# Kernel tuning notes

Hardware: AMD Instinct MI355X
Metric: run time of the kernel (lower is better)

## Reference

```python
import jax, jax.numpy as jnp
import numpy as np

N_NODES = 50000
N_EDGES = 600000
IN_FEAT = 128
OUT_FEAT = 128
NUM_RELS = 8


def setup_inputs() -> dict:
    key = jax.random.key(0)
    ks = jax.random.split(key, 8)
    h = jax.random.normal(ks[0], (N_NODES, IN_FEAT), dtype=jnp.float32)
    # xavier_uniform-like scale for relation weights
    limit = float(np.sqrt(6.0 / (IN_FEAT + OUT_FEAT)))
    weight = jax.random.uniform(ks[1], (NUM_RELS, IN_FEAT, OUT_FEAT), jnp.float32, -limit, limit)
    limit_g = float(np.sqrt(6.0 / (IN_FEAT + 1)))
    gate_weight = jax.random.uniform(ks[2], (NUM_RELS, IN_FEAT, 1), jnp.float32, -limit_g, limit_g)
    h_bias = jnp.zeros((OUT_FEAT,), jnp.float32)
    loop_weight = jax.random.uniform(ks[3], (IN_FEAT, OUT_FEAT), jnp.float32, -limit, limit)
    norm = jax.random.uniform(ks[4], (N_EDGES, 1), jnp.float32)
    src = jax.random.randint(ks[5], (N_EDGES,), 0, N_NODES, dtype=jnp.int32)
    dst = jax.random.randint(ks[6], (N_EDGES,), 0, N_NODES, dtype=jnp.int32)
    rel_type = jax.random.randint(ks[7], (N_EDGES,), 0, NUM_RELS, dtype=jnp.int32)
    return {"h": h, "weight": weight, "gate_weight": gate_weight, "h_bias": h_bias,
            "loop_weight": loop_weight, "norm": norm, "src": src, "dst": dst,
            "rel_type": rel_type}


def reference(h, weight, gate_weight, h_bias, loop_weight, norm, src, dst, rel_type):
    n_nodes = h.shape[0]
    # Transform all nodes under every relation once ([R, N, out]); cheaper than
    # materializing per-edge [E, in, out] weight gathers for small R.
    h_rel = jnp.einsum('ni,rio->rno', h, weight)          # [R, N, out]
    msg = h_rel[rel_type, src]                             # [E, out] gather
    msg = msg * norm                                       # per-edge norm
    # relation-specific scalar gate on src features
    gate_rel = jnp.einsum('ni,ri->rn', h, gate_weight[:, :, 0])  # [R, N]
    gate = jax.nn.sigmoid(gate_rel[rel_type, src])[:, None]      # [E, 1]
    msg = msg * gate
    # scatter-sum messages into destination nodes
    agg = jax.ops.segment_sum(msg, dst, num_segments=n_nodes)    # [N, out]
    out = agg + h_bias + h @ loop_weight                   # bias + self-loop
    out = jax.nn.relu(out)                                 # activation
    # dropout p=0.0 (deterministic) -> identity
    return out
```

## Files before the change

### kernel.cpp

```cpp
#include <hip/hip_runtime.h>

#define N_NODES 50000
#define N_EDGES 600000
#define F 128
#define NRELL 9
#define NB_SCAN 196
#define NB2 1563

#define WT3_OFF   0
#define H2_OFF    294912
#define GATE3_OFF 13094912
#define CNT3_OFF  14694912
#define EXCL3_OFF 16294912
#define BSUM3_OFF 17895168
#define REC3_OFF  17901568
#define A3_OFF    22701568
#define WS_NEED3  ((size_t)138012160)

#define GATE_OFF   294912
#define HREL_OFF   1894912
#define HREL_BYTES (9ll*N_NODES*128*2)
#define CNT_OFF    117094912
#define BASE_OFF   117294912
#define CUR_OFF    117494912
#define BSUM_OFF   117694912
#define SORT_OFF   117695936
#define WS_NEED2   ((size_t)120095936)
#define WS_NEED1   ((size_t)HREL_OFF + (size_t)HREL_BYTES)

typedef __attribute__((ext_vector_type(8))) short short8;
typedef __attribute__((ext_vector_type(4))) float floatx4;

__device__ inline unsigned short f32_to_bf16(float f) {
    unsigned u = __float_as_uint(f);
    unsigned r = u + 0x7fff + ((u >> 16) & 1);
    return (unsigned short)(r >> 16);
}
__device__ inline float bf16_to_f32(unsigned short s) {
    return __uint_as_float(((unsigned)s) << 16);
}
__device__ inline float bf16lo(unsigned m) { return __uint_as_float(m << 16); }
__device__ inline float bf16hi(unsigned m) { return __uint_as_float(m & 0xffff0000u); }
__device__ inline float sigmoidf(float x) { return 1.f / (1.f + __expf(-x)); }

__global__ void k_prep_w(const float* __restrict__ W, const float* __restrict__ LW,
                         unsigned short* __restrict__ Wt, int swz) {
    int idx = blockIdx.x * 256 + threadIdx.x;
    if (idx >= 9 * 128 * 128) return;
    int r = idx >> 14;
    int rem = idx & 16383;
    int i = rem >> 7, o = rem & 127;
    float v = (r < 8) ? W[(r << 14) + (i << 7) + o] : LW[(i << 7) + o];
    int pos;
    if (swz) {
        int g = (i >> 3) ^ (o & 7);
        pos = (r << 14) + (o << 7) + (g << 3) + (i & 7);
    } else {
        pos = (r << 14) + (o << 7) + i;
    }
    Wt[pos] = f32_to_bf16(v);
}

__global__ void k_prep_h(const float* __restrict__ h, const float* __restrict__ gw,
                         unsigned short* __restrict__ h2, float* __restrict__ gate) {
    int wave = threadIdx.x >> 6, lane = threadIdx.x & 63;
    int n = blockIdx.x * 4 + wave;
    float2 hv = *(const float2*)(h + (size_t)n * F + lane * 2);
    unsigned val = (unsigned)f32_to_bf16(hv.x) | ((unsigned)f32_to_bf16(hv.y) << 16);
    *(unsigned*)(h2 + (size_t)n * F + lane * 2) = val;
    #pragma unroll
    for (int r = 0; r < 8; ++r) {
        float2 wv = *(const float2*)(gw + r * F + lane * 2);
        float p = hv.x * wv.x + hv.y * wv.y;
        #pragma unroll
        for (int off = 32; off; off >>= 1) p += __shfl_xor(p, off);
        if (lane == 0) gate[r * N_NODES + n] = sigmoidf(p);
    }
}

__global__ void k_hist2(const int* __restrict__ dst, const int* __restrict__ rel,
                        int* __restrict__ cnt) {
    int e = blockIdx.x * 256 + threadIdx.x;
    if (e < N_EDGES) atomicAdd(&cnt[dst[e] * 8 + rel[e]], 1);
}

__global__ void k_s1(const int* __restrict__ cnt, int* __restrict__ excl,
                     int* __restrict__ bsum) {
    __shared__ int sh[256];
    int g = blockIdx.x * 256 + threadIdx.x;
    int v = (g < 400000) ? cnt[g] : 0;
    sh[threadIdx.x] = v;
    __syncthreads();
    #pragma unroll
    for (int off = 1; off < 256; off <<= 1) {
        int t = (threadIdx.x >= off) ? sh[threadIdx.x - off] : 0;
        __syncthreads();
        sh[threadIdx.x] += t;
        __syncthreads();
    }
    if (g < 400000) excl[g] = sh[threadIdx.x] - v;
    if (threadIdx.x == 255) bsum[blockIdx.x] = sh[255];
}

__global__ void k_s2(int* __restrict__ bsum) {
    __shared__ int sh[256];
    int t = threadIdx.x;
    int v[7];
    int s = 0;
    #pragma unroll
    for (int j = 0; j < 7; ++j) {
        int idx = t * 7 + j;
        v[j] = (idx < NB2) ? bsum[idx] : 0;
        s += v[j];
    }
    sh[t] = s;
    __syncthreads();
    #pragma unroll
    for (int off = 1; off < 256; off <<= 1) {
        int tt = (t >= off) ? sh[t - off] : 0;
        __syncthreads();
        sh[t] += tt;
        __syncthreads();
    }
    int run = sh[t] - s;
    #pragma unroll
    for (int j = 0; j < 7; ++j) {
        int idx = t * 7 + j;
        if (idx < NB2) bsum[idx] = run;
        run += v[j];
    }
}

__global__ void k_s3(int* __restrict__ excl, const int* __restrict__ bsum,
                     int* __restrict__ cursor) {
    int g = blockIdx.x * 256 + threadIdx.x;
    if (g < 400000) {
        int b = excl[g] + bsum[blockIdx.x];
        excl[g] = b;
        cursor[g] = b;
    }
    if (g == 0) excl[400000] = N_EDGES;
}

__global__ void k_scatter2(const int* __restrict__ src, const int* __restrict__ dst,
                           const int* __restrict__ rel, const float* __restrict__ norm,
                           const float* __restrict__ gate, int* __restrict__ cursor,
                           int2* __restrict__ rec) {
    int e = blockIdx.x * 256 + threadIdx.x;
    if (e >= N_EDGES) return;
    int d = dst[e], r = rel[e], s = src[e];
    int pos = atomicAdd(&cursor[d * 8 + r], 1);
    float sc = norm[e] * gate[r * N_NODES + s];
    rec[pos] = make_int2(s, __float_as_int(sc));
}

__global__ __launch_bounds__(256) void k_aggA(const unsigned short* __restrict__ h2,
                                              const int2* __restrict__ rec,
                                              const int* __restrict__ excl,
                                              unsigned short* __restrict__ A) {
    int wave = threadIdx.x >> 6, lane = threadIdx.x & 63;
    int n = blockIdx.x * 4 + wave;
    int ex = 0;
    if (lane < 9) ex = excl[n * 8 + lane];
    int e0 = __shfl(ex, 0), e8 = __shfl(ex, 8);
    int deg = e8 - e0;
    unsigned short* Arow = A + (size_t)n * 1152;
    int swo = (((lane >> 2) ^ (n & 7)) << 2) + (lane & 3);

    if (deg <= 64) {
        int rs = 0; float rsc = 0.f;
        if (lane < deg) {
            int2 rc = rec[e0 + lane];
            rs = rc.x; rsc = __int_as_float(rc.y);
        }
        for (int r = 0; r < 8; ++r) {
            int s = __shfl(ex, r) - e0;
            int e = __shfl(ex, r + 1) - e0;
            float a0 = 0.f, a1 = 0.f;
            for (int j = s; j < e; ++j) {
                int sj = __shfl(rs, j);
                float sc = __shfl(rsc, j);
                unsigned m = *(const unsigned*)(h2 + (size_t)sj * F + lane * 2);
                a0 += sc * bf16lo(m);
                a1 += sc * bf16hi(m);
            }
            unsigned val = (unsigned)f32_to_bf16(a0) | ((unsigned)f32_to_bf16(a1) << 16);
            ((unsigned*)(Arow + r * 128))[swo] = val;
        }
    } else {
        for (int r = 0; r < 8; ++r) {
            int s = __shfl(ex, r);
            int e = __shfl(ex, r + 1);
            float a0 = 0.f, a1 = 0.f;
            for (int idx = s; idx < e; ++idx) {
                int2 rc = rec[idx];
                float sc = __int_as_float(rc.y);
                unsigned m = *(const unsigned*)(h2 + (size_t)rc.x * F + lane * 2);
                a0 += sc * bf16lo(m);
                a1 += sc * bf16hi(m);
            }
            unsigned val = (unsigned)f32_to_bf16(a0) | ((unsigned)f32_to_bf16(a1) << 16);
            ((unsigned*)(Arow + r * 128))[swo] = val;
        }
    }
    unsigned hm = ((const unsigned*)(h2 + (size_t)n * F))[lane];
    ((unsigned*)(Arow + 8 * 128))[swo] = hm;
}

__global__ __launch_bounds__(256) void k_gemmA(const unsigned short* __restrict__ A,
                                               const unsigned short* __restrict__ Wt,
                                               const float* __restrict__ bias,
                                               float* __restrict__ out) {
    __shared__ unsigned short sA[16384];
    __shared__ unsigned short sB[16384];
    int tid = threadIdx.x;
    int nb = blockIdx.x * 128;
    int wave = tid >> 6, lane = tid & 63, lrow = lane & 15, quad = lane >> 4;

    floatx4 acc[2][8];
    #pragma unroll
    for (int mt = 0; mt < 2; ++mt)
        #pragma unroll
        for (int nt = 0; nt < 8; ++nt) acc[mt][nt] = (floatx4){0.f, 0.f, 0.f, 0.f};

    for (int kb = 0; kb < 9; ++kb) {
        __syncthreads();
        #pragma unroll
        for (int it = 0; it < 8; ++it) {
            int g = it * 256 + tid;
            int row = g >> 4, gr = g & 15;
            *(uint4*)(&sA[row * 128 + gr * 8]) =
                *(const uint4*)(A + (size_t)(nb + row) * 1152 + kb * 128 + gr * 8);
            *(uint4*)(&sB[row * 128 + gr * 8]) =
                *(const uint4*)(Wt + (kb << 14) + (g << 3));
        }
        __syncthreads();
        #pragma unroll
        for (int kt = 0; kt < 4; ++kt) {
            int j = kt * 4 + quad;
            int sw = (j ^ (lrow & 7)) << 3;
            short8 a0 = *(const short8*)(&sA[(wave * 32 + lrow) * 128 + sw]);
            short8 a1 = *(const short8*)(&sA[(wave * 32 + 16 + lrow) * 128 + sw]);
            #pragma unroll
            for (int nt = 0; nt < 8; ++nt) {
                short8 b = *(const short8*)(&sB[(nt * 16 + lrow) * 128 + sw]);
                acc[0][nt] = __builtin_amdgcn_mfma_f32_16x16x32_bf16(a0, b, acc[0][nt], 0, 0, 0);
                acc[1][nt] = __builtin_amdgcn_mfma_f32_16x16x32_bf16(a1, b, acc[1][nt], 0, 0, 0);
            }
        }
    }
    #pragma unroll
    for (int mt = 0; mt < 2; ++mt) {
        #pragma unroll
        for (int nt = 0; nt < 8; ++nt) {
            int col = nt * 16 + lrow;
            float bv = bias[col];
            #pragma unroll
            for (int g = 0; g < 4; ++g) {
                int row = nb + wave * 32 + mt * 16 + quad * 4 + g;
                if (row < N_NODES)
                    out[(size_t)row * F + col] = fmaxf(acc[mt][nt][g] + bv, 0.f);
            }
        }
    }
}

__global__ void k_gate(const float* __restrict__ h, const float* __restrict__ gw,
                       float* __restrict__ gate) {
    int wave = threadIdx.x >> 6, lane = threadIdx.x & 63;
    int n = blockIdx.x * 4 + wave;
    if (n >= N_NODES) return;
    float2 hv = *(const float2*)(h + (size_t)n * F + lane * 2);
    #pragma unroll
    for (int r = 0; r < 8; ++r) {
        float2 wv = *(const float2*)(gw + r * F + lane * 2);
        float p = hv.x * wv.x + hv.y * wv.y;
        #pragma unroll
        for (int off = 32; off; off >>= 1) p += __shfl_xor(p, off);
        if (lane == 0) gate[r * N_NODES + n] = sigmoidf(p);
    }
}

#define LDH 136
#define LDW 136
__global__ __launch_bounds__(256) void k_hrel(const float* __restrict__ h,
                                              const unsigned short* __restrict__ Wt,
                                              unsigned short* __restrict__ hrel) {
    __shared__ unsigned short hA[64 * LDH];
    __shared__ unsigned short wB[128 * LDW];
    int tid = threadIdx.x;
    int nb = blockIdx.x * 64;
    #pragma unroll
    for (int it = 0; it < 8; ++it) {
        int idx = it * 1024 + tid * 4;
        int row = idx >> 7, col = idx & 127;
        int node = nb + row;
        float4 v;
        if (node < N_NODES) v = *(const float4*)(h + (size_t)node * F + col);
        else                v = make_float4(0.f, 0.f, 0.f, 0.f);
        ushort4 b;
        b.x = f32_to_bf16(v.x); b.y = f32_to_bf16(v.y);
        b.z = f32_to_bf16(v.z); b.w = f32_to_bf16(v.w);
        *(ushort4*)(&hA[row * LDH + col]) = b;
    }
    int wave = tid >> 6, lane = tid & 63;
    int lrow = lane & 15, quad = lane >> 4;
    const unsigned short* aptr = &hA[(wave * 16 + lrow) * LDH + quad * 8];
    for (int r = 0; r < NRELL; ++r) {
        __syncthreads();
        #pragma unroll
        for (int it = 0; it < 8; ++it) {
            int idx = it * 2048 + tid * 8;
            int o = idx >> 7, i = idx & 127;
            *(uint4*)(&wB[o * LDW + i]) = *(const uint4*)(Wt + (r << 14) + idx);
        }
        __syncthreads();
        floatx4 acc[8];
        #pragma unroll
        for (int nt = 0; nt < 8; ++nt) acc[nt] = (floatx4){0.f, 0.f, 0.f, 0.f};
        #pragma unroll
        for (int kt = 0; kt < 4; ++kt) {
            short8 a = *(const short8*)(aptr + kt * 32);
            #pragma unroll
            for (int nt = 0; nt < 8; ++nt) {
                short8 b = *(const short8*)(&wB[(nt * 16 + lrow) * LDW + kt * 32 + quad * 8]);
                acc[nt] = __builtin_amdgcn_mfma_f32_16x16x32_bf16(a, b, acc[nt], 0, 0, 0);
            }
        }
        unsigned short* dstp = hrel + (size_t)r * N_NODES * F;
        #pragma unroll
        for (int nt = 0; nt < 8; ++nt) {
            #pragma unroll
            for (int g = 0; g < 4; ++g) {
                int node = nb + wave * 16 + quad * 4 + g;
                if (node < N_NODES)
                    dstp[(size_t)node * F + nt * 16 + lrow] = f32_to_bf16(acc[nt][g]);
            }
        }
    }
}

__global__ void k_hist(const int* __restrict__ dst, int* __restrict__ cnt) {
    int e = blockIdx.x * 256 + threadIdx.x;
    if (e < N_EDGES) atomicAdd(&cnt[dst[e]], 1);
}

__global__ void k_scan1(const int* __restrict__ cnt, int* __restrict__ excl,
// ... 105 lines not shown
    float v1 = bf16hi(m) * scale;
    float* op = out + (size_t)d * F + lane * 2;
    unsafeAtomicAdd(op, v0);
    unsafeAtomicAdd(op + 1, v1);
}

__global__ void k_final(float* __restrict__ out, const float* __restrict__ bias,
                        const unsigned short* __restrict__ hrel8) {
    int idx = blockIdx.x * 256 + threadIdx.x;
    if (idx >= N_NODES * 32) return;
    int node = idx >> 5, c4 = (idx & 31) * 4;
    float4 a = *(float4*)(out + (size_t)node * F + c4);
    float4 b = *(const float4*)(bias + c4);
    ushort4 l = *(const ushort4*)(hrel8 + (size_t)node * F + c4);
    float o0 = fmaxf(a.x + b.x + bf16_to_f32(l.x), 0.f);
    float o1 = fmaxf(a.y + b.y + bf16_to_f32(l.y), 0.f);
    float o2 = fmaxf(a.z + b.z + bf16_to_f32(l.z), 0.f);
    float o3 = fmaxf(a.w + b.w + bf16_to_f32(l.w), 0.f);
    *(float4*)(out + (size_t)node * F + c4) = make_float4(o0, o1, o2, o3);
}

__global__ void k_edges_fb(const float* __restrict__ h, const float* __restrict__ W,
                           const float* __restrict__ gw, const float* __restrict__ norm,
                           const int* __restrict__ src, const int* __restrict__ dst,
                           const int* __restrict__ rel, float* __restrict__ out) {
    int wave = threadIdx.x >> 6, lane = threadIdx.x & 63;
    int e = blockIdx.x * 4 + wave;
    if (e >= N_EDGES) return;
    int s = src[e], d = dst[e], r = rel[e];
    float2 hv = *(const float2*)(h + (size_t)s * F + lane * 2);
    float2 gv = *(const float2*)(gw + r * F + lane * 2);
    float p = hv.x * gv.x + hv.y * gv.y;
    #pragma unroll
    for (int off = 32; off; off >>= 1) p += __shfl_xor(p, off);
    float scale = norm[e] * sigmoidf(p);
    const float* wr = W + ((size_t)r << 14);
    float a0 = 0.f, a1 = 0.f;
    for (int i2 = 0; i2 < 64; ++i2) {
        float x0 = __shfl(hv.x, i2), x1 = __shfl(hv.y, i2);
        a0 += x0 * wr[(2 * i2) * F + lane]      + x1 * wr[(2 * i2 + 1) * F + lane];
        a1 += x0 * wr[(2 * i2) * F + 64 + lane] + x1 * wr[(2 * i2 + 1) * F + 64 + lane];
    }
    unsafeAtomicAdd(out + (size_t)d * F + lane,      a0 * scale);
    unsafeAtomicAdd(out + (size_t)d * F + 64 + lane, a1 * scale);
}

__global__ void k_final_fb(const float* __restrict__ h, const float* __restrict__ LW,
                           const float* __restrict__ bias, float* __restrict__ out) {
    int wave = threadIdx.x >> 6, lane = threadIdx.x & 63;
    int n = blockIdx.x * 4 + wave;
    if (n >= N_NODES) return;
    float2 hv = *(const float2*)(h + (size_t)n * F + lane * 2);
    float a0 = 0.f, a1 = 0.f;
    for (int i2 = 0; i2 < 64; ++i2) {
        float x0 = __shfl(hv.x, i2), x1 = __shfl(hv.y, i2);
        a0 += x0 * LW[(2 * i2) * F + lane]      + x1 * LW[(2 * i2 + 1) * F + lane];
        a1 += x0 * LW[(2 * i2) * F + 64 + lane] + x1 * LW[(2 * i2 + 1) * F + 64 + lane];
    }
    float* op = out + (size_t)n * F;
    op[lane]      = fmaxf(op[lane]      + bias[lane]      + a0, 0.f);
    op[64 + lane] = fmaxf(op[64 + lane] + bias[64 + lane] + a1, 0.f);
}

extern "C" void kernel_launch(void* const* d_in, const int* in_sizes, int n_in,
                              void* d_out, int out_size, void* d_ws, size_t ws_size,
                              hipStream_t stream) {
    const float* h    = (const float*)d_in[0];
    const float* W    = (const float*)d_in[1];
    const float* gw   = (const float*)d_in[2];
    const float* bias = (const float*)d_in[3];
    const float* lw   = (const float*)d_in[4];
    const float* norm = (const float*)d_in[5];
    const int* src    = (const int*)d_in[6];
    const int* dst    = (const int*)d_in[7];
    const int* rel    = (const int*)d_in[8];
    float* out = (float*)d_out;

    if (ws_size >= WS_NEED3) {
        unsigned short* Wt   = (unsigned short*)((char*)d_ws + WT3_OFF);
        unsigned short* h2   = (unsigned short*)((char*)d_ws + H2_OFF);
        float*          gate = (float*)((char*)d_ws + GATE3_OFF);
        int*            cnt  = (int*)((char*)d_ws + CNT3_OFF);
        int*            excl = (int*)((char*)d_ws + EXCL3_OFF);
        int*            bsum = (int*)((char*)d_ws + BSUM3_OFF);
        int2*           rec  = (int2*)((char*)d_ws + REC3_OFF);
        unsigned short* A    = (unsigned short*)((char*)d_ws + A3_OFF);

        hipMemsetAsync(cnt, 0, 400000 * sizeof(int), stream);
        k_prep_w<<<576, 256, 0, stream>>>(W, lw, Wt, 1);
        k_prep_h<<<12500, 256, 0, stream>>>(h, gw, h2, gate);
        k_hist2<<<2344, 256, 0, stream>>>(dst, rel, cnt);
        k_s1<<<NB2, 256, 0, stream>>>(cnt, excl, bsum);
        k_s2<<<1, 256, 0, stream>>>(bsum);
        k_s3<<<NB2, 256, 0, stream>>>(excl, bsum, cnt);
        k_scatter2<<<2344, 256, 0, stream>>>(src, dst, rel, norm, gate, cnt, rec);
        k_aggA<<<12500, 256, 0, stream>>>(h2, rec, excl, A);
        k_gemmA<<<391, 256, 0, stream>>>(A, Wt, bias, out);
    } else if (ws_size >= WS_NEED2) {
        unsigned short* Wt   = (unsigned short*)d_ws;
        float*          gate = (float*)((char*)d_ws + GATE_OFF);
        unsigned short* hrel = (unsigned short*)((char*)d_ws + HREL_OFF);
        int* cnt    = (int*)((char*)d_ws + CNT_OFF);
        int* base   = (int*)((char*)d_ws + BASE_OFF);
        int* cursor = (int*)((char*)d_ws + CUR_OFF);
        int* bsum   = (int*)((char*)d_ws + BSUM_OFF);
        int* sorted = (int*)((char*)d_ws + SORT_OFF);
        hipMemsetAsync(cnt, 0, N_NODES * sizeof(int), stream);
        k_prep_w<<<576, 256, 0, stream>>>(W, lw, Wt, 0);
        k_gate<<<12500, 256, 0, stream>>>(h, gw, gate);
        k_hist<<<2344, 256, 0, stream>>>(dst, cnt);
        k_scan1<<<NB_SCAN, 256, 0, stream>>>(cnt, base, bsum);
        k_scan2<<<1, 256, 0, stream>>>(bsum);
        k_scan3<<<NB_SCAN, 256, 0, stream>>>(base, bsum, cursor);
        k_scatter<<<2344, 256, 0, stream>>>(dst, cursor, sorted);
        k_hrel<<<782, 256, 0, stream>>>(h, Wt, hrel);
        k_agg<<<12500, 256, 0, stream>>>(hrel, gate, norm, src, rel, sorted,
                                         base, cnt, bias, out);
    } else if (ws_size >= WS_NEED1) {
        unsigned short* Wt   = (unsigned short*)d_ws;
        float*          gate = (float*)((char*)d_ws + GATE_OFF);
        unsigned short* hrel = (unsigned short*)((char*)d_ws + HREL_OFF);
        hipMemsetAsync(d_out, 0, (size_t)out_size * sizeof(float), stream);
        k_prep_w<<<576, 256, 0, stream>>>(W, lw, Wt, 0);
        k_gate<<<12500, 256, 0, stream>>>(h, gw, gate);
        k_hrel<<<782, 256, 0, stream>>>(h, Wt, hrel);
        k_edges<<<150000, 256, 0, stream>>>(hrel, gate, norm, src, dst, rel, out);
        k_final<<<6250, 256, 0, stream>>>(out, bias, hrel + (size_t)8 * N_NODES * F);
    } else {
        hipMemsetAsync(d_out, 0, (size_t)out_size * sizeof(float), stream);
        k_edges_fb<<<150000, 256, 0, stream>>>(h, W, gw, norm, src, dst, rel, out);
        k_final_fb<<<12500, 256, 0, stream>>>(h, lw, bias, out);
    }
}
```

Measured before the change: 272.0 us.

## Fuse prep kernels with memset and replace three-pass scan with single-pass decoupled scan

Folds the count memset, weight conversion and node conversion/gate kernels into one multi-role launch that also zeroes the scan metadata. Replaces the three-kernel block scan (local scan, single-block bsum scan, add-back) with one 49-block chained scan. That scan takes block ids from an atomic ticket and passes prefixes between blocks through flag words, spin-waiting on the previous block. The goal is fewer launches and fewer passes over the 400K-entry count array, at the cost of a serial inter-block chain across only 49 blocks.

```diff
diff --git a/kernel.cpp b/kernel.cpp
--- a/kernel.cpp
+++ b/kernel.cpp
@@ -6,6 +6,7 @@
 #define NRELL 9
 #define NB_SCAN 196
 #define NB2 1563
+#define SCB 49
 
 #define WT3_OFF   0
 #define H2_OFF    294912
@@ -42,6 +43,240 @@
 __device__ inline float bf16lo(unsigned m) { return __uint_as_float(m << 16); }
 __device__ inline float bf16hi(unsigned m) { return __uint_as_float(m & 0xffff0000u); }
 __device__ inline float sigmoidf(float x) { return 1.f / (1.f + __expf(-x)); }
+__device__ inline unsigned packbf(float a0, float a1) {
+    return (unsigned)f32_to_bf16(a0) | ((unsigned)f32_to_bf16(a1) << 16);
+}
+
+__global__ __launch_bounds__(256) void k_prep(
+    const float* __restrict__ h, const float* __restrict__ W,
+    const float* __restrict__ gw, const float* __restrict__ lw,
+    unsigned short* __restrict__ Wt, unsigned short* __restrict__ h2,
+    float* __restrict__ gate, int* __restrict__ cnt, int* __restrict__ meta)
+{
+    int vb = blockIdx.x, tid = threadIdx.x;
+    if (vb < 391) {
+        int idx = vb * 1024 + tid * 4;
+        if (idx < 400000) *(int4*)(cnt + idx) = make_int4(0, 0, 0, 0);
+    } else if (vb == 391) {
+        meta[tid] = 0;
+    } else if (vb < 968) {
+        int idx = (vb - 392) * 256 + tid;
+        int r = idx >> 14, rem = idx & 16383, i = rem >> 7, o = rem & 127;
+        float v = (r < 8) ? W[(r << 14) + (i << 7) + o] : lw[(i << 7) + o];
+        int g = (i >> 3) ^ (o & 7);
+        Wt[(r << 14) + (o << 7) + (g << 3) + (i & 7)] = f32_to_bf16(v);
+    } else {
+        int wave = tid >> 6, lane = tid & 63;
+        int n = (vb - 968) * 4 + wave;
+        float2 hv = *(const float2*)(h + (size_t)n * F + lane * 2);
+        *(unsigned*)(h2 + (size_t)n * F + lane * 2) = packbf(hv.x, hv.y);
+        #pragma unroll
+        for (int r = 0; r < 8; ++r) {
+            float2 wv = *(const float2*)(gw + r * F + lane * 2);
+            float p = hv.x * wv.x + hv.y * wv.y;
+            #pragma unroll
+            for (int off = 32; off; off >>= 1) p += __shfl_xor(p, off);
+            if (lane == 0) gate[r * N_NODES + n] = sigmoidf(p);
+        }
+    }
+}
+
+__global__ void k_hist2(const int* __restrict__ dst, const int* __restrict__ rel,
+                        int* __restrict__ cnt) {
+    int e = blockIdx.x * 256 + threadIdx.x;
+    if (e < N_EDGES) atomicAdd(&cnt[dst[e] * 8 + rel[e]], 1);
+}
+
+__global__ __launch_bounds__(256) void k_scan(int* __restrict__ cnt,
+                                              int* __restrict__ excl,
+                                              int* __restrict__ meta) {
+    __shared__ int sh[256];
+    __shared__ int sbid, sprefix;
+    int tid = threadIdx.x;
+    if (tid == 0) sbid = atomicAdd(&meta[0], 1);
+    __syncthreads();
+    int bid = sbid;
+    int* flagsum = meta + 16;
+
+    int g0 = bid * 8192 + tid * 32;
+    int vals[32];
+    #pragma unroll
+    for (int j = 0; j < 8; ++j) {
+        int idx = g0 + j * 4;
+        int4 v = (idx + 3 < 400000) ? *(const int4*)(cnt + idx)
+                                    : make_int4(idx < 400000 ? cnt[idx] : 0,
+                                                idx + 1 < 400000 ? cnt[idx + 1] : 0,
+                                                idx + 2 < 400000 ? cnt[idx + 2] : 0,
+                                                idx + 3 < 400000 ? cnt[idx + 3] : 0);
+        vals[j * 4] = v.x; vals[j * 4 + 1] = v.y; vals[j * 4 + 2] = v.z; vals[j * 4 + 3] = v.w;
+    }
+    int run = 0;
+    #pragma unroll
+    for (int j = 0; j < 32; ++j) { int e = run; run += vals[j]; vals[j] = e; }
+    int tsum = run;
+
+    sh[tid] = tsum;
+    __syncthreads();
+    #pragma unroll
+    for (int off = 1; off < 256; off <<= 1) {
+        int t = (tid >= off) ? sh[tid - off] : 0;
+        __syncthreads();
+        sh[tid] += t;
+        __syncthreads();
+    }
+    int texcl = sh[tid] - tsum;
+    int btot = sh[255];
+
+    if (tid == 0) {
+        int prefix = 0;
+        if (bid > 0) {
+            int f;
+            do {
+                f = __hip_atomic_load(&flagsum[bid - 1], __ATOMIC_ACQUIRE,
+                                      __HIP_MEMORY_SCOPE_AGENT);
+                if (f == 0) __builtin_amdgcn_s_sleep(1);
+            } while (f == 0);
+            prefix = f - 1;
+        }
+        sprefix = prefix;
+        __hip_atomic_store(&flagsum[bid], prefix + btot + 1, __ATOMIC_RELEASE,
+                           __HIP_MEMORY_SCOPE_AGENT);
+    }
+    __syncthreads();
+    int p = sprefix + texcl;
+
+    #pragma unroll
+    for (int j = 0; j < 32; ++j) {
+        int idx = g0 + j;
+        if (idx < 400000) {
+            int b = p + vals[j];
+            excl[idx] = b;
+            cnt[idx] = b;
+        }
+    }
+    if (bid == SCB - 1 && tid == 0) excl[400000] = N_EDGES;
+}
+
+__global__ void k_scatter2(const int* __restrict__ src, const int* __restrict__ dst,
+                           const int* __restrict__ rel, const float* __restrict__ norm,
+                           const float* __restrict__ gate, int* __restrict__ cursor,
+                           int2* __restrict__ rec) {
+    int e = blockIdx.x * 256 + threadIdx.x;
+    if (e >= N_EDGES) return;
+    int d = dst[e], r = rel[e], s = src[e];
+    int pos = atomicAdd(&cursor[d * 8 + r], 1);
+    float sc = norm[e] * gate[r * N_NODES + s];
+    rec[pos] = make_int2(s, __float_as_int(sc));
+}
+
+__global__ __launch_bounds__(256) void k_aggA(const unsigned short* __restrict__ h2,
+                                              const int2* __restrict__ rec,
+                                              const int* __restrict__ excl,
+                                              unsigned short* __restrict__ A) {
+    int wave = threadIdx.x >> 6, lane = threadIdx.x & 63;
+    int n = blockIdx.x * 4 + wave;
+    int ex = 0;
+    if (lane < 9) ex = excl[n * 8 + lane];
+    int e0 = __shfl(ex, 0), e8 = __shfl(ex, 8);
+    int deg = e8 - e0;
+    unsigned short* Arow = A + (size_t)n * 1152;
+    int swo = (((lane >> 2) ^ (n & 7)) << 2) + (lane & 3);
+
+    if (deg <= 64) {
+        int rs = 0; float rsc = 0.f;
+        if (lane < deg) {
+            int2 rc = rec[e0 + lane];
+            rs = rc.x; rsc = __int_as_float(rc.y);
+        }
+        for (int r = 0; r < 8; ++r) {
+            int s = __shfl(ex, r) - e0;
+            int e = __shfl(ex, r + 1) - e0;
+            float a0 = 0.f, a1 = 0.f;
+            for (int j = s; j < e; ++j) {
+                int sj = __shfl(rs, j);
+                float sc = __shfl(rsc, j);
+                unsigned m = *(const unsigned*)(h2 + (size_t)sj * F + lane * 2);
+                a0 += sc * bf16lo(m);
+                a1 += sc * bf16hi(m);
+            }
+            ((unsigned*)(Arow + r * 128))[swo] = packbf(a0, a1);
+        }
+    } else {
+        for (int r = 0; r < 8; ++r) {
+            int s = __shfl(ex, r);
+            int e = __shfl(ex, r + 1);
+            float a0 = 0.f, a1 = 0.f;
+            for (int idx = s; idx < e; ++idx) {
+                int2 rc = rec[idx];
+                float sc = __int_as_float(rc.y);
+                unsigned m = *(const unsigned*)(h2 + (size_t)rc.x * F + lane * 2);
+                a0 += sc * bf16lo(m);
+                a1 += sc * bf16hi(m);
+            }
+            ((unsigned*)(Arow + r * 128))[swo] = packbf(a0, a1);
+        }
+    }
+    unsigned hm = ((const unsigned*)(h2 + (size_t)n * F))[lane];
+    ((unsigned*)(Arow + 8 * 128))[swo] = hm;
+}
+
+__global__ __launch_bounds__(256) void k_gemmA(const unsigned short* __restrict__ A,
+                                               const unsigned short* __restrict__ Wt,
+                                               const float* __restrict__ bias,
+                                               float* __restrict__ out) {
+    __shared__ unsigned short sA[16384];
+    __shared__ unsigned short sB[16384];
+    int tid = threadIdx.x;
+    int nb = blockIdx.x * 128;
+    int wave = tid >> 6, lane = tid & 63, lrow = lane & 15, quad = lane >> 4;
+
+    floatx4 acc[2][8];
+    #pragma unroll
+    for (int mt = 0; mt < 2; ++mt)
+        #pragma unroll
+        for (int nt = 0; nt < 8; ++nt) acc[mt][nt] = (floatx4){0.f, 0.f, 0.f, 0.f};
+
+    for (int kb = 0; kb < 9; ++kb) {
+        __syncthreads();
+        #pragma unroll
+        for (int it = 0; it < 8; ++it) {
+            int g = it * 256 + tid;
+            int row = g >> 4, gr = g & 15;
+            *(uint4*)(&sA[row * 128 + gr * 8]) =
+                *(const uint4*)(A + (size_t)(nb + row) * 1152 + kb * 128 + gr * 8);
+            *(uint4*)(&sB[row * 128 + gr * 8]) =
+                *(const uint4*)(Wt + (kb << 14) + (g << 3));
+        }
+        __syncthreads();
+        #pragma unroll
+        for (int kt = 0; kt < 4; ++kt) {
+            int j = kt * 4 + quad;
+            int sw = (j ^ (lrow & 7)) << 3;
+            short8 a0 = *(const short8*)(&sA[(wave * 32 + lrow) * 128 + sw]);
+            short8 a1 = *(const short8*)(&sA[(wave * 32 + 16 + lrow) * 128 + sw]);
+            #pragma unroll
+            for (int nt = 0; nt < 8; ++nt) {
+                short8 b = *(const short8*)(&sB[(nt * 16 + lrow) * 128 + sw]);
+                acc[0][nt] = __builtin_amdgcn_mfma_f32_16x16x32_bf16(a0, b, acc[0][nt], 0, 0, 0);
+                acc[1][nt] = __builtin_amdgcn_mfma_f32_16x16x32_bf16(a1, b, acc[1][nt], 0, 0, 0);
+            }
+        }
+    }
+    #pragma unroll
+    for (int mt = 0; mt < 2; ++mt) {
+        #pragma unroll
+        for (int nt = 0; nt < 8; ++nt) {
+            int col = nt * 16 + lrow;
+            float bv = bias[col];
+            #pragma unroll
+            for (int g = 0; g < 4; ++g) {
+                int row = nb + wave * 32 + mt * 16 + quad * 4 + g;
+                if (row < N_NODES)
+                    out[(size_t)row * F + col] = fmaxf(acc[mt][nt][g] + bv, 0.f);
+            }
+        }
+    }
+}
 
 __global__ void k_prep_w(const float* __restrict__ W, const float* __restrict__ LW,
                          unsigned short* __restrict__ Wt, int swz) {
@@ -59,210 +294,6 @@
         pos = (r << 14) + (o << 7) + i;
     }
     Wt[pos] = f32_to_bf16(v);
-}
-
-__global__ void k_prep_h(const float* __restrict__ h, const float* __restrict__ gw,
-                         unsigned short* __restrict__ h2, float* __restrict__ gate) {
-    int wave = threadIdx.x >> 6, lane = threadIdx.x & 63;
-    int n = blockIdx.x * 4 + wave;
-    float2 hv = *(const float2*)(h + (size_t)n * F + lane * 2);
-    unsigned val = (unsigned)f32_to_bf16(hv.x) | ((unsigned)f32_to_bf16(hv.y) << 16);
-    *(unsigned*)(h2 + (size_t)n * F + lane * 2) = val;
-    #pragma unroll
-    for (int r = 0; r < 8; ++r) {
-        float2 wv = *(const float2*)(gw + r * F + lane * 2);
-        float p = hv.x * wv.x + hv.y * wv.y;
-        #pragma unroll
-        for (int off = 32; off; off >>= 1) p += __shfl_xor(p, off);
-        if (lane == 0) gate[r * N_NODES + n] = sigmoidf(p);
-    }
-}
-
-__global__ void k_hist2(const int* __restrict__ dst, const int* __restrict__ rel,
-                        int* __restrict__ cnt) {
-    int e = blockIdx.x * 256 + threadIdx.x;
-    if (e < N_EDGES) atomicAdd(&cnt[dst[e] * 8 + rel[e]], 1);
-}
-
-__global__ void k_s1(const int* __restrict__ cnt, int* __restrict__ excl,
-                     int* __restrict__ bsum) {
-    __shared__ int sh[256];
-    int g = blockIdx.x * 256 + threadIdx.x;
-    int v = (g < 400000) ? cnt[g] : 0;
-    sh[threadIdx.x] = v;
-    __syncthreads();
-    #pragma unroll
-    for (int off = 1; off < 256; off <<= 1) {
-        int t = (threadIdx.x >= off) ? sh[threadIdx.x - off] : 0;
-        __syncthreads();
-        sh[threadIdx.x] += t;
-        __syncthreads();
-    }
-    if (g < 400000) excl[g] = sh[threadIdx.x] - v;
-    if (threadIdx.x == 255) bsum[blockIdx.x] = sh[255];
-}
-
-__global__ void k_s2(int* __restrict__ bsum) {
-    __shared__ int sh[256];
-    int t = threadIdx.x;
-    int v[7];
-    int s = 0;
-    #pragma unroll
-    for (int j = 0; j < 7; ++j) {
-        int idx = t * 7 + j;
-        v[j] = (idx < NB2) ? bsum[idx] : 0;
-        s += v[j];
-    }
-    sh[t] = s;
-    __syncthreads();
-    #pragma unroll
-    for (int off = 1; off < 256; off <<= 1) {
-        int tt = (t >= off) ? sh[t - off] : 0;
-        __syncthreads();
-        sh[t] += tt;
-        __syncthreads();
-    }
-    int run = sh[t] - s;
-    #pragma unroll
-    for (int j = 0; j < 7; ++j) {
-        int idx = t * 7 + j;
-        if (idx < NB2) bsum[idx] = run;
-        run += v[j];
-    }
-}
-
-__global__ void k_s3(int* __restrict__ excl, const int* __restrict__ bsum,
-                     int* __restrict__ cursor) {
-    int g = blockIdx.x * 256 + threadIdx.x;
-    if (g < 400000) {
-        int b = excl[g] + bsum[blockIdx.x];
-        excl[g] = b;
-        cursor[g] = b;
-    }
-    if (g == 0) excl[400000] = N_EDGES;
-}
-
-__global__ void k_scatter2(const int* __restrict__ src, const int* __restrict__ dst,
-                           const int* __restrict__ rel, const float* __restrict__ norm,
-                           const float* __restrict__ gate, int* __restrict__ cursor,
-                           int2* __restrict__ rec) {
-    int e = blockIdx.x * 256 + threadIdx.x;
-    if (e >= N_EDGES) return;
-    int d = dst[e], r = rel[e], s = src[e];
-    int pos = atomicAdd(&cursor[d * 8 + r], 1);
-    float sc = norm[e] * gate[r * N_NODES + s];
-    rec[pos] = make_int2(s, __float_as_int(sc));
-}
-
-__global__ __launch_bounds__(256) void k_aggA(const unsigned short* __restrict__ h2,
-                                              const int2* __restrict__ rec,
-                                              const int* __restrict__ excl,
-                                              unsigned short* __restrict__ A) {
-    int wave = threadIdx.x >> 6, lane = threadIdx.x & 63;
-    int n = blockIdx.x * 4 + wave;
-    int ex = 0;
-    if (lane < 9) ex = excl[n * 8 + lane];
-    int e0 = __shfl(ex, 0), e8 = __shfl(ex, 8);
-    int deg = e8 - e0;
-    unsigned short* Arow = A + (size_t)n * 1152;
-    int swo = (((lane >> 2) ^ (n & 7)) << 2) + (lane & 3);
-
-    if (deg <= 64) {
-        int rs = 0; float rsc = 0.f;
-        if (lane < deg) {
-            int2 rc = rec[e0 + lane];
-            rs = rc.x; rsc = __int_as_float(rc.y);
-        }
-        for (int r = 0; r < 8; ++r) {
-            int s = __shfl(ex, r) - e0;
-            int e = __shfl(ex, r + 1) - e0;
-            float a0 = 0.f, a1 = 0.f;
-            for (int j = s; j < e; ++j) {
-                int sj = __shfl(rs, j);
-                float sc = __shfl(rsc, j);
-                unsigned m = *(const unsigned*)(h2 + (size_t)sj * F + lane * 2);
-                a0 += sc * bf16lo(m);
-                a1 += sc * bf16hi(m);
-            }
-            unsigned val = (unsigned)f32_to_bf16(a0) | ((unsigned)f32_to_bf16(a1) << 16);
-            ((unsigned*)(Arow + r * 128))[swo] = val;
-        }
-    } else {
-        for (int r = 0; r < 8; ++r) {
-            int s = __shfl(ex, r);
-            int e = __shfl(ex, r + 1);
-            float a0 = 0.f, a1 = 0.f;
-            for (int idx = s; idx < e; ++idx) {
-                int2 rc = rec[idx];
-                float sc = __int_as_float(rc.y);
-                unsigned m = *(const unsigned*)(h2 + (size_t)rc.x * F + lane * 2);
-                a0 += sc * bf16lo(m);
-                a1 += sc * bf16hi(m);
-            }
-            unsigned val = (unsigned)f32_to_bf16(a0) | ((unsigned)f32_to_bf16(a1) << 16);
-            ((unsigned*)(Arow + r * 128))[swo] = val;
-        }
-    }
-    unsigned hm = ((const unsigned*)(h2 + (size_t)n * F))[lane];
-    ((unsigned*)(Arow + 8 * 128))[swo] = hm;
-}
-
-__global__ __launch_bounds__(256) void k_gemmA(const unsigned short* __restrict__ A,
-                                               const unsigned short* __restrict__ Wt,
-                                               const float* __restrict__ bias,
-                                               float* __restrict__ out) {
-    __shared__ unsigned short sA[16384];
-    __shared__ unsigned short sB[16384];
-    int tid = threadIdx.x;
-    int nb = blockIdx.x * 128;
-    int wave = tid >> 6, lane = tid & 63, lrow = lane & 15, quad = lane >> 4;
-
-    floatx4 acc[2][8];
-    #pragma unroll
-    for (int mt = 0; mt < 2; ++mt)
-        #pragma unroll
-        for (int nt = 0; nt < 8; ++nt) acc[mt][nt] = (floatx4){0.f, 0.f, 0.f, 0.f};
-
-    for (int kb = 0; kb < 9; ++kb) {
-        __syncthreads();
-        #pragma unroll
-        for (int it = 0; it < 8; ++it) {
-            int g = it * 256 + tid;
-            int row = g >> 4, gr = g & 15;
-            *(uint4*)(&sA[row * 128 + gr * 8]) =
-                *(const uint4*)(A + (size_t)(nb + row) * 1152 + kb * 128 + gr * 8);
-            *(uint4*)(&sB[row * 128 + gr * 8]) =
-                *(const uint4*)(Wt + (kb << 14) + (g << 3));
-        }
-        __syncthreads();
-        #pragma unroll
-        for (int kt = 0; kt < 4; ++kt) {
-            int j = kt * 4 + quad;
-            int sw = (j ^ (lrow & 7)) << 3;
-            short8 a0 = *(const short8*)(&sA[(wave * 32 + lrow) * 128 + sw]);
-            short8 a1 = *(const short8*)(&sA[(wave * 32 + 16 + lrow) * 128 + sw]);
-            #pragma unroll
-            for (int nt = 0; nt < 8; ++nt) {
-                short8 b = *(const short8*)(&sB[(nt * 16 + lrow) * 128 + sw]);
-                acc[0][nt] = __builtin_amdgcn_mfma_f32_16x16x32_bf16(a0, b, acc[0][nt], 0, 0, 0);
-                acc[1][nt] = __builtin_amdgcn_mfma_f32_16x16x32_bf16(a1, b, acc[1][nt], 0, 0, 0);
-            }
-        }
-    }
-    #pragma unroll
-    for (int mt = 0; mt < 2; ++mt) {
-        #pragma unroll
-        for (int nt = 0; nt < 8; ++nt) {
-            int col = nt * 16 + lrow;
-            float bv = bias[col];
-            #pragma unroll
-            for (int g = 0; g < 4; ++g) {
-                int row = nb + wave * 32 + mt * 16 + quad * 4 + g;
-                if (row < N_NODES)
-                    out[(size_t)row * F + col] = fmaxf(acc[mt][nt][g] + bv, 0.f);
-            }
-        }
-    }
 }
 
 __global__ void k_gate(const float* __restrict__ h, const float* __restrict__ gw,
@@ -534,17 +565,13 @@
         float*          gate = (float*)((char*)d_ws + GATE3_OFF);
         int*            cnt  = (int*)((char*)d_ws + CNT3_OFF);
         int*            excl = (int*)((char*)d_ws + EXCL3_OFF);
-        int*            bsum = (int*)((char*)d_ws + BSUM3_OFF);
+        int*            meta = (int*)((char*)d_ws + BSUM3_OFF);
         int2*           rec  = (int2*)((char*)d_ws + REC3_OFF);
         unsigned short* A    = (unsigned short*)((char*)d_ws + A3_OFF);
 
-        hipMemsetAsync(cnt, 0, 400000 * sizeof(int), stream);
-        k_prep_w<<<576, 256, 0, stream>>>(W, lw, Wt, 1);
-        k_prep_h<<<12500, 256, 0, stream>>>(h, gw, h2, gate);
+        k_prep<<<13468, 256, 0, stream>>>(h, W, gw, lw, Wt, h2, gate, cnt, meta);
         k_hist2<<<2344, 256, 0, stream>>>(dst, rel, cnt);
-        k_s1<<<NB2, 256, 0, stream>>>(cnt, excl, bsum);
-        k_s2<<<1, 256, 0, stream>>>(bsum);
-        k_s3<<<NB2, 256, 0, stream>>>(excl, bsum, cnt);
+        k_scan<<<SCB, 256, 0, stream>>>(cnt, excl, meta);
         k_scatter2<<<2344, 256, 0, stream>>>(src, dst, rel, norm, gate, cnt, rec);
         k_aggA<<<12500, 256, 0, stream>>>(h2, rec, excl, A);
         k_gemmA<<<391, 256, 0, stream>>>(A, Wt, bias, out);
```

Measured after the change: 318.9 us. 17.2% more time.

## Fuse prep kernels, transpose gate layout, read self-loop features directly in GEMM

Applied to the files above, without the earlier changes.

Merges weight conversion, bf16 feature conversion with gate computation, and the edge histogram into one launch that branches on block index, removing two kernel launches. The gate table moves from relation-major to node-major, so each node's eight gates are stored contiguously and scatter reads per source node are local. The aggregation kernel no longer copies each node's own features into a ninth slot of A, and the GEMM loads the self-loop tile straight from h2 with an on-the-fly swizzle. This shrinks the A buffer and the workspace requirement, at the cost of a branch in the GEMM load loop.

```diff
diff --git a/kernel.cpp b/kernel.cpp
--- a/kernel.cpp
+++ b/kernel.cpp
@@ -15,7 +15,7 @@
 #define BSUM3_OFF 17895168
 #define REC3_OFF  17901568
 #define A3_OFF    22701568
-#define WS_NEED3  ((size_t)138012160)
+#define WS_NEED3  ((size_t)125199872)
 
 #define GATE_OFF   294912
 #define HREL_OFF   1894912
@@ -42,6 +42,234 @@
 __device__ inline float bf16lo(unsigned m) { return __uint_as_float(m << 16); }
 __device__ inline float bf16hi(unsigned m) { return __uint_as_float(m & 0xffff0000u); }
 __device__ inline float sigmoidf(float x) { return 1.f / (1.f + __expf(-x)); }
+__device__ inline unsigned packbf(float a0, float a1) {
+    return (unsigned)f32_to_bf16(a0) | ((unsigned)f32_to_bf16(a1) << 16);
+}
+
+__global__ __launch_bounds__(256) void k_prep(
+    const float* __restrict__ h, const float* __restrict__ W,
+    const float* __restrict__ gw, const float* __restrict__ lw,
+    const int* __restrict__ dst, const int* __restrict__ rel,
+    unsigned short* __restrict__ Wt, unsigned short* __restrict__ h2,
+    float* __restrict__ gate, int* __restrict__ cnt)
+{
+    int vb = blockIdx.x, tid = threadIdx.x;
+    if (vb < 576) {
+        int idx = vb * 256 + tid;
+        int r = idx >> 14, rem = idx & 16383, i = rem >> 7, o = rem & 127;
+        float v = (r < 8) ? W[(r << 14) + (i << 7) + o] : lw[(i << 7) + o];
+        int g = (i >> 3) ^ (o & 7);
+        Wt[(r << 14) + (o << 7) + (g << 3) + (i & 7)] = f32_to_bf16(v);
+    } else if (vb < 13076) {
+        int wave = tid >> 6, lane = tid & 63;
+        int n = (vb - 576) * 4 + wave;
+        float2 hv = *(const float2*)(h + (size_t)n * F + lane * 2);
+        *(unsigned*)(h2 + (size_t)n * F + lane * 2) = packbf(hv.x, hv.y);
+        float g = 0.f;
+        #pragma unroll
+        for (int r = 0; r < 8; ++r) {
+            float2 wv = *(const float2*)(gw + r * F + lane * 2);
+            float p = hv.x * wv.x + hv.y * wv.y;
+            #pragma unroll
+            for (int off = 32; off; off >>= 1) p += __shfl_xor(p, off);
+            if (lane == r) g = sigmoidf(p);
+        }
+        if (lane < 8) gate[(size_t)n * 8 + lane] = g;
+    } else {
+        int e = (vb - 13076) * 256 + tid;
+        if (e < N_EDGES) atomicAdd(&cnt[dst[e] * 8 + rel[e]], 1);
+    }
+}
+
+__global__ void k_s1(const int* __restrict__ cnt, int* __restrict__ excl,
+                     int* __restrict__ bsum) {
+    __shared__ int sh[256];
+    int g = blockIdx.x * 256 + threadIdx.x;
+    int v = (g < 400000) ? cnt[g] : 0;
+    sh[threadIdx.x] = v;
+    __syncthreads();
+    #pragma unroll
+    for (int off = 1; off < 256; off <<= 1) {
+        int t = (threadIdx.x >= off) ? sh[threadIdx.x - off] : 0;
+        __syncthreads();
+        sh[threadIdx.x] += t;
+        __syncthreads();
+    }
+    if (g < 400000) excl[g] = sh[threadIdx.x] - v;
+    if (threadIdx.x == 255) bsum[blockIdx.x] = sh[255];
+}
+
+__global__ void k_s2(int* __restrict__ bsum) {
+    __shared__ int sh[256];
+    int t = threadIdx.x;
+    int v[7];
+    int s = 0;
+    #pragma unroll
+    for (int j = 0; j < 7; ++j) {
+        int idx = t * 7 + j;
+        v[j] = (idx < NB2) ? bsum[idx] : 0;
+        s += v[j];
+    }
+    sh[t] = s;
+    __syncthreads();
+    #pragma unroll
+    for (int off = 1; off < 256; off <<= 1) {
+        int tt = (t >= off) ? sh[t - off] : 0;
+        __syncthreads();
+        sh[t] += tt;
+        __syncthreads();
+    }
+    int run = sh[t] - s;
+    #pragma unroll
+    for (int j = 0; j < 7; ++j) {
+        int idx = t * 7 + j;
+        if (idx < NB2) bsum[idx] = run;
+        run += v[j];
+    }
+}
+
+__global__ void k_s3(int* __restrict__ excl, const int* __restrict__ bsum,
+                     int* __restrict__ cursor) {
+    int g = blockIdx.x * 256 + threadIdx.x;
+    if (g < 400000) {
+        int b = excl[g] + bsum[blockIdx.x];
+        excl[g] = b;
+        cursor[g] = b;
+    }
+    if (g == 0) excl[400000] = N_EDGES;
+}
+
+__global__ void k_scatter2(const int* __restrict__ src, const int* __restrict__ dst,
+                           const int* __restrict__ rel, const float* __restrict__ norm,
+                           const float* __restrict__ gate, int* __restrict__ cursor,
+                           int2* __restrict__ rec) {
+    int e = blockIdx.x * 256 + threadIdx.x;
+    if (e >= N_EDGES) return;
+    int d = dst[e], r = rel[e], s = src[e];
+    int pos = atomicAdd(&cursor[d * 8 + r], 1);
+    float sc = norm[e] * gate[(size_t)s * 8 + r];
+    rec[pos] = make_int2(s, __float_as_int(sc));
+}
+
+__global__ __launch_bounds__(256) void k_aggA(const unsigned short* __restrict__ h2,
+                                              const int2* __restrict__ rec,
+                                              const int* __restrict__ excl,
+                                              unsigned short* __restrict__ A) {
+    int wave = threadIdx.x >> 6, lane = threadIdx.x & 63;
+    int n = blockIdx.x * 4 + wave;
+    int ex = 0;
+    if (lane < 9) ex = excl[n * 8 + lane];
+    int e0 = __shfl(ex, 0), e8 = __shfl(ex, 8);
+    int deg = e8 - e0;
+    unsigned short* Arow = A + (size_t)n * 1024;
+    int swo = (((lane >> 2) ^ (n & 7)) << 2) + (lane & 3);
+
+    if (deg <= 64) {
+        int rs = 0; float rsc = 0.f;
+        if (lane < deg) {
+            int2 rc = rec[e0 + lane];
+            rs = rc.x; rsc = __int_as_float(rc.y);
+        }
+        for (int r = 0; r < 8; ++r) {
+            int s = __shfl(ex, r) - e0;
+            int e = __shfl(ex, r + 1) - e0;
+            float a0 = 0.f, a1 = 0.f;
+            for (int j = s; j < e; ++j) {
+                int sj = __shfl(rs, j);
+                float sc = __shfl(rsc, j);
+                unsigned m = *(const unsigned*)(h2 + (size_t)sj * F + lane * 2);
+                a0 += sc * bf16lo(m);
+                a1 += sc * bf16hi(m);
+            }
+            ((unsigned*)(Arow + r * 128))[swo] = packbf(a0, a1);
+        }
+    } else {
+        for (int r = 0; r < 8; ++r) {
+            int s = __shfl(ex, r);
+            int e = __shfl(ex, r + 1);
+            float a0 = 0.f, a1 = 0.f;
+            for (int idx = s; idx < e; ++idx) {
+                int2 rc = rec[idx];
+                float sc = __int_as_float(rc.y);
+                unsigned m = *(const unsigned*)(h2 + (size_t)rc.x * F + lane * 2);
+                a0 += sc * bf16lo(m);
+                a1 += sc * bf16hi(m);
+            }
+            ((unsigned*)(Arow + r * 128))[swo] = packbf(a0, a1);
+        }
+    }
+}
+
+__global__ __launch_bounds__(256) void k_gemmA(const unsigned short* __restrict__ A,
+                                               const unsigned short* __restrict__ h2,
+                                               const unsigned short* __restrict__ Wt,
+                                               const float* __restrict__ bias,
+                                               float* __restrict__ out) {
+    __shared__ unsigned short sA[16384];
+    __shared__ unsigned short sB[16384];
+    int tid = threadIdx.x;
+    int nb = blockIdx.x * 128;
+    int wave = tid >> 6, lane = tid & 63, lrow = lane & 15, quad = lane >> 4;
+
+    floatx4 acc[2][8];
+    #pragma unroll
+    for (int mt = 0; mt < 2; ++mt)
+        #pragma unroll
+        for (int nt = 0; nt < 8; ++nt) acc[mt][nt] = (floatx4){0.f, 0.f, 0.f, 0.f};
+
+    for (int kb = 0; kb < 9; ++kb) {
+        __syncthreads();
+        if (kb < 8) {
+            #pragma unroll
+            for (int it = 0; it < 8; ++it) {
+                int g = it * 256 + tid;
+                int row = g >> 4, gr = g & 15;
+                *(uint4*)(&sA[row * 128 + gr * 8]) =
+                    *(const uint4*)(A + (size_t)(nb + row) * 1024 + kb * 128 + gr * 8);
+                *(uint4*)(&sB[row * 128 + gr * 8]) =
+                    *(const uint4*)(Wt + (kb << 14) + (g << 3));
+            }
+        } else {
+            #pragma unroll
+            for (int it = 0; it < 8; ++it) {
+                int g = it * 256 + tid;
+                int row = g >> 4, gr = g & 15;
+                *(uint4*)(&sA[row * 128 + (gr ^ (row & 7)) * 8]) =
+                    *(const uint4*)(h2 + (size_t)(nb + row) * F + gr * 8);
+                *(uint4*)(&sB[row * 128 + gr * 8]) =
+                    *(const uint4*)(Wt + (kb << 14) + (g << 3));
+            }
+        }
+        __syncthreads();
+        #pragma unroll
+        for (int kt = 0; kt < 4; ++kt) {
+            int j = kt * 4 + quad;
+            int sw = (j ^ (lrow & 7)) << 3;
+            short8 a0 = *(const short8*)(&sA[(wave * 32 + lrow) * 128 + sw]);
+            short8 a1 = *(const short8*)(&sA[(wave * 32 + 16 + lrow) * 128 + sw]);
+            #pragma unroll
+            for (int nt = 0; nt < 8; ++nt) {
+                short8 b = *(const short8*)(&sB[(nt * 16 + lrow) * 128 + sw]);
+                acc[0][nt] = __builtin_amdgcn_mfma_f32_16x16x32_bf16(a0, b, acc[0][nt], 0, 0, 0);
+                acc[1][nt] = __builtin_amdgcn_mfma_f32_16x16x32_bf16(a1, b, acc[1][nt], 0, 0, 0);
+            }
+        }
+    }
+    #pragma unroll
+    for (int mt = 0; mt < 2; ++mt) {
+        #pragma unroll
+        for (int nt = 0; nt < 8; ++nt) {
+            int col = nt * 16 + lrow;
+            float bv = bias[col];
+            #pragma unroll
+            for (int g = 0; g < 4; ++g) {
+                int row = nb + wave * 32 + mt * 16 + quad * 4 + g;
+                if (row < N_NODES)
+                    out[(size_t)row * F + col] = fmaxf(acc[mt][nt][g] + bv, 0.f);
+            }
+        }
+    }
+}
 
 __global__ void k_prep_w(const float* __restrict__ W, const float* __restrict__ LW,
                          unsigned short* __restrict__ Wt, int swz) {
@@ -59,210 +287,6 @@
         pos = (r << 14) + (o << 7) + i;
     }
     Wt[pos] = f32_to_bf16(v);
-}
-
-__global__ void k_prep_h(const float* __restrict__ h, const float* __restrict__ gw,
-                         unsigned short* __restrict__ h2, float* __restrict__ gate) {
-    int wave = threadIdx.x >> 6, lane = threadIdx.x & 63;
-    int n = blockIdx.x * 4 + wave;
-    float2 hv = *(const float2*)(h + (size_t)n * F + lane * 2);
-    unsigned val = (unsigned)f32_to_bf16(hv.x) | ((unsigned)f32_to_bf16(hv.y) << 16);
-    *(unsigned*)(h2 + (size_t)n * F + lane * 2) = val;
-    #pragma unroll
-    for (int r = 0; r < 8; ++r) {
-        float2 wv = *(const float2*)(gw + r * F + lane * 2);
-        float p = hv.x * wv.x + hv.y * wv.y;
-        #pragma unroll
-        for (int off = 32; off; off >>= 1) p += __shfl_xor(p, off);
-        if (lane == 0) gate[r * N_NODES + n] = sigmoidf(p);
-    }
-}
-
-__global__ void k_hist2(const int* __restrict__ dst, const int* __restrict__ rel,
-                        int* __restrict__ cnt) {
-    int e = blockIdx.x * 256 + threadIdx.x;
-    if (e < N_EDGES) atomicAdd(&cnt[dst[e] * 8 + rel[e]], 1);
-}
-
-__global__ void k_s1(const int* __restrict__ cnt, int* __restrict__ excl,
-                     int* __restrict__ bsum) {
-    __shared__ int sh[256];
-    int g = blockIdx.x * 256 + threadIdx.x;
-    int v = (g < 400000) ? cnt[g] : 0;
-    sh[threadIdx.x] = v;
-    __syncthreads();
-    #pragma unroll
-    for (int off = 1; off < 256; off <<= 1) {
-        int t = (threadIdx.x >= off) ? sh[threadIdx.x - off] : 0;
-        __syncthreads();
-        sh[threadIdx.x] += t;
-        __syncthreads();
-    }
-    if (g < 400000) excl[g] = sh[threadIdx.x] - v;
-    if (threadIdx.x == 255) bsum[blockIdx.x] = sh[255];
-}
-
-__global__ void k_s2(int* __restrict__ bsum) {
-    __shared__ int sh[256];
-    int t = threadIdx.x;
-    int v[7];
-    int s = 0;
-    #pragma unroll
-    for (int j = 0; j < 7; ++j) {
-        int idx = t * 7 + j;
-        v[j] = (idx < NB2) ? bsum[idx] : 0;
-        s += v[j];
-    }
-    sh[t] = s;
-    __syncthreads();
-    #pragma unroll
-    for (int off = 1; off < 256; off <<= 1) {
-        int tt = (t >= off) ? sh[t - off] : 0;
-        __syncthreads();
-        sh[t] += tt;
-        __syncthreads();
-    }
-    int run = sh[t] - s;
-    #pragma unroll
-    for (int j = 0; j < 7; ++j) {
-        int idx = t * 7 + j;
-        if (idx < NB2) bsum[idx] = run;
-        run += v[j];
-    }
-}
-
-__global__ void k_s3(int* __restrict__ excl, const int* __restrict__ bsum,
-                     int* __restrict__ cursor) {
-    int g = blockIdx.x * 256 + threadIdx.x;
-    if (g < 400000) {
-        int b = excl[g] + bsum[blockIdx.x];
-        excl[g] = b;
-        cursor[g] = b;
-    }
-    if (g == 0) excl[400000] = N_EDGES;
-}
-
-__global__ void k_scatter2(const int* __restrict__ src, const int* __restrict__ dst,
-                           const int* __restrict__ rel, const float* __restrict__ norm,
-                           const float* __restrict__ gate, int* __restrict__ cursor,
-                           int2* __restrict__ rec) {
-    int e = blockIdx.x * 256 + threadIdx.x;
-    if (e >= N_EDGES) return;
-    int d = dst[e], r = rel[e], s = src[e];
-    int pos = atomicAdd(&cursor[d * 8 + r], 1);
-    float sc = norm[e] * gate[r * N_NODES + s];
-    rec[pos] = make_int2(s, __float_as_int(sc));
-}
-
-__global__ __launch_bounds__(256) void k_aggA(const unsigned short* __restrict__ h2,
-                                              const int2* __restrict__ rec,
-                                              const int* __restrict__ excl,
-                                              unsigned short* __restrict__ A) {
-    int wave = threadIdx.x >> 6, lane = threadIdx.x & 63;
-    int n = blockIdx.x * 4 + wave;
-    int ex = 0;
-    if (lane < 9) ex = excl[n * 8 + lane];
-    int e0 = __shfl(ex, 0), e8 = __shfl(ex, 8);
-    int deg = e8 - e0;
-    unsigned short* Arow = A + (size_t)n * 1152;
-    int swo = (((lane >> 2) ^ (n & 7)) << 2) + (lane & 3);
-
-    if (deg <= 64) {
-        int rs = 0; float rsc = 0.f;
-        if (lane < deg) {
-            int2 rc = rec[e0 + lane];
-            rs = rc.x; rsc = __int_as_float(rc.y);
-        }
-        for (int r = 0; r < 8; ++r) {
-            int s = __shfl(ex, r) - e0;
-            int e = __shfl(ex, r + 1) - e0;
-            float a0 = 0.f, a1 = 0.f;
-            for (int j = s; j < e; ++j) {
-                int sj = __shfl(rs, j);
-                float sc = __shfl(rsc, j);
-                unsigned m = *(const unsigned*)(h2 + (size_t)sj * F + lane * 2);
-                a0 += sc * bf16lo(m);
-                a1 += sc * bf16hi(m);
-            }
-            unsigned val = (unsigned)f32_to_bf16(a0) | ((unsigned)f32_to_bf16(a1) << 16);
-            ((unsigned*)(Arow + r * 128))[swo] = val;
-        }
-    } else {
-        for (int r = 0; r < 8; ++r) {
-            int s = __shfl(ex, r);
-            int e = __shfl(ex, r + 1);
-            float a0 = 0.f, a1 = 0.f;
-            for (int idx = s; idx < e; ++idx) {
-                int2 rc = rec[idx];
-                float sc = __int_as_float(rc.y);
-                unsigned m = *(const unsigned*)(h2 + (size_t)rc.x * F + lane * 2);
-                a0 += sc * bf16lo(m);
-                a1 += sc * bf16hi(m);
-            }
-            unsigned val = (unsigned)f32_to_bf16(a0) | ((unsigned)f32_to_bf16(a1) << 16);
-            ((unsigned*)(Arow + r * 128))[swo] = val;
-        }
-    }
-    unsigned hm = ((const unsigned*)(h2 + (size_t)n * F))[lane];
-    ((unsigned*)(Arow + 8 * 128))[swo] = hm;
-}
-
-__global__ __launch_bounds__(256) void k_gemmA(const unsigned short* __restrict__ A,
-                                               const unsigned short* __restrict__ Wt,
-                                               const float* __restrict__ bias,
-                                               float* __restrict__ out) {
-    __shared__ unsigned short sA[16384];
-    __shared__ unsigned short sB[16384];
-    int tid = threadIdx.x;
-    int nb = blockIdx.x * 128;
-    int wave = tid >> 6, lane = tid & 63, lrow = lane & 15, quad = lane >> 4;
-
-    floatx4 acc[2][8];
-    #pragma unroll
-    for (int mt = 0; mt < 2; ++mt)
-        #pragma unroll
-        for (int nt = 0; nt < 8; ++nt) acc[mt][nt] = (floatx4){0.f, 0.f, 0.f, 0.f};
-
-    for (int kb = 0; kb < 9; ++kb) {
-        __syncthreads();
-        #pragma unroll
-        for (int it = 0; it < 8; ++it) {
-            int g = it * 256 + tid;
-            int row = g >> 4, gr = g & 15;
-            *(uint4*)(&sA[row * 128 + gr * 8]) =
-                *(const uint4*)(A + (size_t)(nb + row) * 1152 + kb * 128 + gr * 8);
-            *(uint4*)(&sB[row * 128 + gr * 8]) =
-                *(const uint4*)(Wt + (kb << 14) + (g << 3));
-        }
-        __syncthreads();
-        #pragma unroll
-        for (int kt = 0; kt < 4; ++kt) {
-            int j = kt * 4 + quad;
-            int sw = (j ^ (lrow & 7)) << 3;
-            short8 a0 = *(const short8*)(&sA[(wave * 32 + lrow) * 128 + sw]);
-            short8 a1 = *(const short8*)(&sA[(wave * 32 + 16 + lrow) * 128 + sw]);
-            #pragma unroll
-            for (int nt = 0; nt < 8; ++nt) {
-                short8 b = *(const short8*)(&sB[(nt * 16 + lrow) * 128 + sw]);
-                acc[0][nt] = __builtin_amdgcn_mfma_f32_16x16x32_bf16(a0, b, acc[0][nt], 0, 0, 0);
-                acc[1][nt] = __builtin_amdgcn_mfma_f32_16x16x32_bf16(a1, b, acc[1][nt], 0, 0, 0);
-            }
-        }
-    }
-    #pragma unroll
-    for (int mt = 0; mt < 2; ++mt) {
-        #pragma unroll
-        for (int nt = 0; nt < 8; ++nt) {
-            int col = nt * 16 + lrow;
-            float bv = bias[col];
-            #pragma unroll
-            for (int g = 0; g < 4; ++g) {
-                int row = nb + wave * 32 + mt * 16 + quad * 4 + g;
-                if (row < N_NODES)
-                    out[(size_t)row * F + col] = fmaxf(acc[mt][nt][g] + bv, 0.f);
-            }
-        }
-    }
 }
 
 __global__ void k_gate(const float* __restrict__ h, const float* __restrict__ gw,
@@ -539,15 +563,13 @@
         unsigned short* A    = (unsigned short*)((char*)d_ws + A3_OFF);
 
         hipMemsetAsync(cnt, 0, 400000 * sizeof(int), stream);
-        k_prep_w<<<576, 256, 0, stream>>>(W, lw, Wt, 1);
-        k_prep_h<<<12500, 256, 0, stream>>>(h, gw, h2, gate);
-        k_hist2<<<2344, 256, 0, stream>>>(dst, rel, cnt);
+        k_prep<<<15420, 256, 0, stream>>>(h, W, gw, lw, dst, rel, Wt, h2, gate, cnt);
         k_s1<<<NB2, 256, 0, stream>>>(cnt, excl, bsum);
         k_s2<<<1, 256, 0, stream>>>(bsum);
         k_s3<<<NB2, 256, 0, stream>>>(excl, bsum, cnt);
         k_scatter2<<<2344, 256, 0, stream>>>(src, dst, rel, norm, gate, cnt, rec);
         k_aggA<<<12500, 256, 0, stream>>>(h2, rec, excl, A);
-        k_gemmA<<<391, 256, 0, stream>>>(A, Wt, bias, out);
+        k_gemmA<<<391, 256, 0, stream>>>(A, h2, Wt, bias, out);
     } else if (ws_size >= WS_NEED2) {
         unsigned short* Wt   = (unsigned short*)d_ws;
         float*          gate = (float*)((char*)d_ws + GATE_OFF);
```

Result: slower. 284.0 us (+4.4%).
